# Optimization experiments

Measured on AMD Instinct MI355X. Metric: run time of the kernel, lower is better.

## Reference

```python
import jax, jax.numpy as jnp
import numpy as np

B, N, C, H = 4, 2048, 1024, 16
D = C // H  # dim_per_head = 64
NEG = -1e9  # stands in for -inf masked_fill (finite to keep grads clean)


def setup_inputs() -> dict:
    key0 = jax.random.key(0)
    ks = jax.random.split(key0, 12)
    inp = {
        "query": jax.random.normal(ks[0], (B, N, C), dtype=jnp.float32),
        "key": jax.random.normal(ks[1], (B, N, C), dtype=jnp.float32),
        "value": jax.random.normal(ks[2], (B, N, C), dtype=jnp.float32),
        "ratio": jax.random.uniform(ks[3], (B, N), dtype=jnp.float32),
        "attn_mask": jax.random.randint(ks[4], (B, N, N), 0, 2) == 1,
        # learned params (Linear layers are bias-free; weights stored as [in, out])
        "Wq": jax.random.normal(ks[5], (C, C), dtype=jnp.float32) / np.sqrt(C),
        "Wk": jax.random.normal(ks[6], (C, C), dtype=jnp.float32) / np.sqrt(C),
        "Wv": jax.random.normal(ks[7], (C, C), dtype=jnp.float32) / np.sqrt(C),
        "Wo": jax.random.normal(ks[8], (C, C), dtype=jnp.float32) / np.sqrt(C),
        "gamma": jnp.ones((C,), dtype=jnp.float32),
        "beta": jnp.zeros((C,), dtype=jnp.float32),
    }
    return inp


def reference(query, key, value, ratio, attn_mask, Wq, Wk, Wv, Wo, gamma, beta):
    residual = query
    # projections -> [B, H, N, D]
    q = (query @ Wq).reshape(B, N, H, D).transpose(0, 2, 1, 3)
    k = (key @ Wk).reshape(B, N, H, D).transpose(0, 2, 1, 3)
    v = (value @ Wv).reshape(B, N, H, D).transpose(0, 2, 1, 3)

    scale = D ** (-0.5)
    scores = jnp.einsum("bhid,bhjd->bhij", q, k) * scale  # [B,H,N1,N2]
    scores = jnp.where(attn_mask[:, None, :, :], NEG, scores)
    scores = scores * ratio[:, None, None, :]  # ratio broadcast over heads & queries
    # NON-STANDARD: softmax over dim=2 (the QUERY axis), faithful to source
    attn = jax.nn.softmax(scores, axis=2)
    # dropout omitted (eval mode)
    ctx = jnp.einsum("bhij,bhjd->bhid", attn, v)  # [B,H,N1,D]
    ctx = ctx.transpose(0, 2, 1, 3).reshape(B, N, C)
    out = ctx @ Wo
    x = residual + out
    # LayerNorm over last dim
    mu = jnp.mean(x, axis=-1, keepdims=True)
    var = jnp.var(x, axis=-1, keepdims=True)
    xn = (x - mu) * jax.lax.rsqrt(var + 1e-5)
    return xn * gamma + beta
```

## Files before the change

### kernel.cpp

```cpp
#include <hip/hip_runtime.h>
#include <hip/hip_bf16.h>
#include <stdint.h>

#define BB 4
#define NN 2048
#define CC 1024
#define HH 16
#define DD 64

typedef __attribute__((ext_vector_type(8))) short bf16x8;
typedef __attribute__((ext_vector_type(4))) float f32x4;

#define LOG2E 1.44269504088896f

__device__ __forceinline__ float exp2_hw(float x) {
  float r;
  asm("v_exp_f32 %0, %1" : "=v"(r) : "v"(x));
  return r;
}
#define EXP2(x) exp2_hw(x)

__device__ __forceinline__ unsigned short f2bf(float x) {
  uint32_t u = __float_as_uint(x);
  uint32_t r = (u + 0x7FFFu + ((u >> 16) & 1u)) >> 16;
  return (unsigned short)r;
}
__device__ __forceinline__ float bf2f(unsigned short v) {
  return __uint_as_float(((uint32_t)v) << 16);
}
__device__ __forceinline__ float load_in_f(const void* p, size_t idx, int f32in) {
  if (f32in) return ((const float*)p)[idx];
  return bf2f(((const uint16_t*)p)[idx]);
}
__device__ __forceinline__ void gload16(uint16_t* lds_base, const uint16_t* gsrc) {
  __builtin_amdgcn_global_load_lds(
      (const __attribute__((address_space(1))) uint32_t*)(const void*)gsrc,
      (__attribute__((address_space(3))) uint32_t*)(void*)lds_base,
      16, 0, 0);
}

__global__ void detect_kernel(const uint32_t* __restrict__ q,
                              const uint32_t* __restrict__ m,
                              int* __restrict__ flags) {
  if (threadIdx.x == 0 && blockIdx.x == 0) {
    int sane = 0;
    for (int i = 0; i < 128; ++i) {
      uint32_t w = q[i];
      int e0 = (int)((w >> 7) & 0xFFu);
      int e1 = (int)((w >> 23) & 0xFFu);
      sane += (e0 >= 0x70 && e0 <= 0x8F) ? 1 : 0;
      sane += (e1 >= 0x70 && e1 <= 0x8F) ? 1 : 0;
    }
    flags[0] = (sane >= 208) ? 0 : 1;
    int allsmall = 1;
    for (int i = 0; i < 16; ++i) if (m[i] > 1u) allsmall = 0;
    flags[1] = allsmall;
  }
}

__global__ void prep_kernel(const void* __restrict__ s0, const void* __restrict__ s1,
                            const void* __restrict__ s2, const void* __restrict__ ratio,
                            const void* __restrict__ mask,
                            uint16_t* __restrict__ d0, uint16_t* __restrict__ d1,
                            uint16_t* __restrict__ d2,
                            float* __restrict__ rs, float* __restrict__ ng,
                            uint32_t* __restrict__ mb, const int* __restrict__ flags) {
  const int z = blockIdx.z;
  if (z < 3) {
    const int f32in = flags[0];
    const void* src = (z == 0) ? s0 : (z == 1) ? s1 : s2;
    uint16_t* dst = (z == 0) ? d0 : (z == 1) ? d1 : d2;
    int idx = blockIdx.x * blockDim.x + threadIdx.x;
    const int total = (BB * NN * CC) >> 2;
    const int stride = gridDim.x * blockDim.x;
    if (f32in) {
      const float4* s = (const float4*)src;
      for (; idx < total; idx += stride) {
        float4 v = s[idx];
        ushort4 o;
        o.x = f2bf(v.x); o.y = f2bf(v.y); o.z = f2bf(v.z); o.w = f2bf(v.w);
        ((ushort4*)dst)[idx] = o;
      }
    } else {
      const ushort4* s = (const ushort4*)src;
      for (; idx < total; idx += stride) ((ushort4*)dst)[idx] = s[idx];
    }
  } else if (z == 3) {
    const int isint = flags[1];
    const int gw = (blockIdx.x * blockDim.x + threadIdx.x) >> 6;
    const int lane = threadIdx.x & 63;
    const int nw = (gridDim.x * blockDim.x) >> 6;
    const int totalw = (BB * NN * NN) >> 6;
    for (int w = gw; w < totalw; w += nw) {
      int e = w * 64 + lane;
      bool m;
      if (isint) m = (((const int*)mask)[e] != 0);
      else       m = (((const uint8_t*)mask)[e] != 0);
      unsigned long long bal = __ballot(m);
      if (lane == 0) ((unsigned long long*)mb)[w] = bal;
    }
  } else {
    const int f32in = flags[0];
    int idx = blockIdx.x * blockDim.x + threadIdx.x;
    if (idx < BB * NN) {
      float r = load_in_f(ratio, idx, f32in);
      rs[idx] = r * 0.125f * LOG2E;
      ng[idx] = r * (-1e9f) * LOG2E;
    }
  }
}

__global__ __launch_bounds__(256)
void transW(const void* w0, const void* w1, const void* w2, const void* w3,
            uint16_t* __restrict__ wt, const int* __restrict__ flags) {
  const int f32in = flags[0];
  const void* src = (blockIdx.z == 0) ? w0 : (blockIdx.z == 1) ? w1
                   : (blockIdx.z == 2) ? w2 : w3;
  uint16_t* dst = wt + (size_t)blockIdx.z * CC * CC;
  __shared__ float t[32][33];
  const int tx = threadIdx.x, ty = threadIdx.y;
  const int n0 = blockIdx.x * 32, k0 = blockIdx.y * 32;
#pragma unroll
  for (int r = 0; r < 4; ++r) {
    int k = k0 + ty + r * 8;
    t[ty + r * 8][tx] = load_in_f(src, (size_t)k * CC + n0 + tx, f32in);
  }
  __syncthreads();
#pragma unroll
  for (int r = 0; r < 4; ++r) {
    int n = n0 + ty + r * 8;
    dst[(size_t)n * CC + k0 + tx] = f2bf(t[tx][ty + r * 8]);
  }
}

__global__ __launch_bounds__(256, 2)
void gemmQKV(const uint16_t* __restrict__ xq, const uint16_t* __restrict__ xk,
             const uint16_t* __restrict__ xv, const uint16_t* __restrict__ Wt,
             uint16_t* __restrict__ qb, uint16_t* __restrict__ kb,
             uint16_t* __restrict__ vtb, const float* __restrict__ rowscale) {
  __shared__ uint16_t As[128 * 32];
  __shared__ uint16_t Bs[128 * 32];
  const int tid = threadIdx.x;
  const int wid = tid >> 6, lane = tid & 63;
  const int g = lane >> 4, c = lane & 15;
  const int n0g = blockIdx.y * 128;
  const int sel = n0g >> 10;
  const int n0 = n0g & 1023;
  const int m0 = blockIdx.x * 128;
  const uint16_t* A = (sel == 0) ? xq : (sel == 1) ? xk : xv;
  const uint16_t* Bt = Wt + (size_t)sel * CC * CC;
  const int wr = wid >> 1, wc = wid & 1;
  f32x4 acc[4][4] = {};
  for (int k0 = 0; k0 < 1024; k0 += 32) {
    __syncthreads();
#pragma unroll
    for (int is = 0; is < 2; ++is) {
      int sb = is * 256 + wid * 64;
      int s = sb + lane;
      int r = s >> 2, kp = s & 3;
      int kps = kp ^ ((r >> 1) & 3);
      gload16(&As[sb * 8], A + (size_t)(m0 + r) * 1024 + k0 + kps * 8);
      gload16(&Bs[sb * 8], Bt + (size_t)(n0 + r) * 1024 + k0 + kps * 8);
    }
    __syncthreads();
    bf16x8 a[4], b[4];
#pragma unroll
    for (int mi = 0; mi < 4; ++mi) {
      int row = wr * 64 + mi * 16 + c;
      a[mi] = *(const bf16x8*)&As[row * 32 + (g ^ ((row >> 1) & 3)) * 8];
    }
#pragma unroll
    for (int ni = 0; ni < 4; ++ni) {
      int row = wc * 64 + ni * 16 + c;
      b[ni] = *(const bf16x8*)&Bs[row * 32 + (g ^ ((row >> 1) & 3)) * 8];
    }
#pragma unroll
    for (int mi = 0; mi < 4; ++mi)
#pragma unroll
      for (int ni = 0; ni < 4; ++ni)
        acc[mi][ni] = __builtin_amdgcn_mfma_f32_16x16x32_bf16(a[mi], b[ni], acc[mi][ni], 0, 0, 0);
  }
  float rsv[4][4];
  if (sel == 1) {
#pragma unroll
    for (int mi = 0; mi < 4; ++mi)
#pragma unroll
      for (int r = 0; r < 4; ++r)
        rsv[mi][r] = rowscale[m0 + wr * 64 + mi * 16 + g * 4 + r];
  }
#pragma unroll
  for (int mi = 0; mi < 4; ++mi)
#pragma unroll
    for (int ni = 0; ni < 4; ++ni)
#pragma unroll
      for (int r = 0; r < 4; ++r) {
        int mrow = m0 + wr * 64 + mi * 16 + g * 4 + r;
        int ncol = n0 + wc * 64 + ni * 16 + c;
        float v = acc[mi][ni][r];
        int b_ = mrow >> 11, i = mrow & 2047, h = ncol >> 6, d = ncol & 63;
        if (sel == 0) {
          qb[((size_t)(b_ * 16 + h) * 2048 + i) * 64 + d] = f2bf(v);
        } else if (sel == 1) {
          kb[((size_t)(b_ * 16 + h) * 2048 + i) * 64 + d] = f2bf(v * rsv[mi][r]);
        } else {
          vtb[((size_t)(b_ * 16 + h) * 64 + d) * 2048 + i] = f2bf(v);
        }
      }
}

__global__ __launch_bounds__(256, 2)
void gemmO(const uint16_t* __restrict__ A, const uint16_t* __restrict__ Bt,
           float* __restrict__ out, const void* __restrict__ resid,
           const int* __restrict__ flags) {
  __shared__ uint16_t As[128 * 32];
  __shared__ uint16_t Bs[128 * 32];
  const int tid = threadIdx.x;
  const int wid = tid >> 6, lane = tid & 63;
  const int g = lane >> 4, c = lane & 15;
  const int m0 = blockIdx.x * 128, n0 = blockIdx.y * 128;
  const int wr = wid >> 1, wc = wid & 1;
  f32x4 acc[4][4] = {};
  for (int k0 = 0; k0 < 1024; k0 += 32) {
    __syncthreads();
#pragma unroll
    for (int is = 0; is < 2; ++is) {
      int sb = is * 256 + wid * 64;
      int s = sb + lane;
      int r = s >> 2, kp = s & 3;
      int kps = kp ^ ((r >> 1) & 3);
      gload16(&As[sb * 8], A + (size_t)(m0 + r) * 1024 + k0 + kps * 8);
      gload16(&Bs[sb * 8], Bt + (size_t)(n0 + r) * 1024 + k0 + kps * 8);
    }
    __syncthreads();
    bf16x8 a[4], b[4];
#pragma unroll
    for (int mi = 0; mi < 4; ++mi) {
      int row = wr * 64 + mi * 16 + c;
      a[mi] = *(const bf16x8*)&As[row * 32 + (g ^ ((row >> 1) & 3)) * 8];
    }
#pragma unroll
    for (int ni = 0; ni < 4; ++ni) {
      int row = wc * 64 + ni * 16 + c;
      b[ni] = *(const bf16x8*)&Bs[row * 32 + (g ^ ((row >> 1) & 3)) * 8];
    }
#pragma unroll
    for (int mi = 0; mi < 4; ++mi)
#pragma unroll
      for (int ni = 0; ni < 4; ++ni)
        acc[mi][ni] = __builtin_amdgcn_mfma_f32_16x16x32_bf16(a[mi], b[ni], acc[mi][ni], 0, 0, 0);
  }
  const int f32in = flags[0];
#pragma unroll
  for (int mi = 0; mi < 4; ++mi)
#pragma unroll
    for (int ni = 0; ni < 4; ++ni)
#pragma unroll
      for (int r = 0; r < 4; ++r) {
        int mrow = m0 + wr * 64 + mi * 16 + g * 4 + r;
        int ncol = n0 + wc * 64 + ni * 16 + c;
        size_t idx = (size_t)mrow * 1024 + ncol;
        out[idx] = acc[mi][ni][r] + load_in_f(resid, idx, f32in);
      }
}

__global__ __launch_bounds__(256, 2)
void attn_stats(const uint16_t* __restrict__ qb, const uint16_t* __restrict__ kb,
                uint16_t* __restrict__ vt, const uint32_t* __restrict__ mbits,
                const float* __restrict__ ngbuf) {
  __shared__ float redL[4][128];
  __shared__ float invsh[128];
  const int tid = threadIdx.x, wid = tid >> 6, lane = tid & 63;
  const int g = lane >> 4, c = lane & 15;
  const int bh = blockIdx.x, b_ = bh >> 4;
  const int j0 = blockIdx.y * 128;
  const uint16_t* Kg = kb + (size_t)bh * NN * DD + (size_t)j0 * DD;
  const uint16_t* Qg = qb + (size_t)bh * NN * DD;
  const uint32_t* Mrow = mbits + (size_t)b_ * NN * 64 + (j0 >> 5);
  bf16x8 kf[2][8];
#pragma unroll
  for (int ks = 0; ks < 2; ++ks)
#pragma unroll
    for (int nj = 0; nj < 8; ++nj)
      kf[ks][nj] = *(const bf16x8*)(Kg + (size_t)(nj * 16 + c) * 64 + ks * 32 + g * 8);
  float ng8[8], l_[8];
#pragma unroll
  for (int nj = 0; nj < 8; ++nj) {
    ng8[nj] = ngbuf[b_ * NN + j0 + nj * 16 + c];
    l_[nj] = 0.f;
  }
  bf16x8 qa[2][2], qn[2][2];
  uint4 mqa[8], mqb[8];
#pragma unroll
  for (int ks = 0; ks < 2; ++ks)
#pragma unroll
    for (int mi = 0; mi < 2; ++mi)
      qa[ks][mi] = *(const bf16x8*)(Qg + (size_t)(wid * 32 + mi * 16 + c) * 64 + ks * 32 + g * 8);
#pragma unroll
  for (int u = 0; u < 8; ++u) {
    int mi = u >> 2, r = u & 3;
    mqa[u] = *(const uint4*)(Mrow + (size_t)(wid * 32 + mi * 16 + g * 4 + r) * 64);
  }

  auto body = [&](bf16x8 (&qc)[2][2], bf16x8 (&qp)[2][2],
                  uint4 (&mc)[8], uint4 (&mn)[8], int i0) {
    f32x4 sacc[2][8] = {};
    __builtin_amdgcn_s_setprio(1);
#pragma unroll
    for (int ks = 0; ks < 2; ++ks)
#pragma unroll
      for (int mi = 0; mi < 2; ++mi)
#pragma unroll
        for (int nj = 0; nj < 8; ++nj)
          sacc[mi][nj] = __builtin_amdgcn_mfma_f32_16x16x32_bf16(qc[ks][mi], kf[ks][nj], sacc[mi][nj], 0, 0, 0);
    __builtin_amdgcn_s_setprio(0);
    int ip = (i0 + 128) & (NN - 1);
#pragma unroll
    for (int ks = 0; ks < 2; ++ks)
#pragma unroll
      for (int mi = 0; mi < 2; ++mi)
        qp[ks][mi] = *(const bf16x8*)(Qg + (size_t)(ip + wid * 32 + mi * 16 + c) * 64 + ks * 32 + g * 8);
#pragma unroll
    for (int u = 0; u < 8; ++u) {
      int mi = u >> 2, r = u & 3;
      mn[u] = *(const uint4*)(Mrow + (size_t)(ip + wid * 32 + mi * 16 + g * 4 + r) * 64);
    }
#pragma unroll
    for (int mi = 0; mi < 2; ++mi)
#pragma unroll
      for (int r = 0; r < 4; ++r) {
        const uint4 mw = mc[mi * 4 + r];
#pragma unroll
        for (int nj = 0; nj < 8; ++nj) {
          uint32_t w = (nj < 2) ? mw.x : (nj < 4) ? mw.y : (nj < 6) ? mw.z : mw.w;
          bool bit = (w >> ((nj & 1) * 16 + c)) & 1u;
          float se = bit ? ng8[nj] : sacc[mi][nj][r];
          l_[nj] += EXP2(se);
        }
      }
  };
  for (int it = 0; it < 8; ++it) {
    body(qa, qn, mqa, mqb, it * 256);
    body(qn, qa, mqb, mqa, it * 256 + 128);
  }
#pragma unroll
  for (int nj = 0; nj < 8; ++nj) {
    float l = l_[nj];
    l += __shfl_xor(l, 16);
    l += __shfl_xor(l, 32);
    if (g == 0) redL[wid][nj * 16 + c] = l;
  }
  __syncthreads();
  if (tid < 128) {
    float L = redL[0][tid] + redL[1][tid] + redL[2][tid] + redL[3][tid];
    invsh[tid] = 1.0f / L;
  }
  __syncthreads();
  {
    const int d = tid >> 2, jseg = (tid & 3) * 32;
    uint16_t* vrow = vt + (size_t)bh * DD * NN + (size_t)d * NN + j0 + jseg;
#pragma unroll
    for (int u = 0; u < 4; ++u) {
      bf16x8 v = *(const bf16x8*)(vrow + u * 8);
      bf16x8 o;
#pragma unroll
      for (int e = 0; e < 8; ++e) {
        float f = bf2f((unsigned short)v[e]) * invsh[jseg + u * 8 + e];
        o[e] = (short)f2bf(f);
      }
      *(bf16x8*)(vrow + u * 8) = o;
    }
  }
}

__global__ __launch_bounds__(256, 3)
void attn_pv(const uint16_t* __restrict__ qb, const uint16_t* __restrict__ kb,
             const uint16_t* __restrict__ vt, const uint32_t* __restrict__ mbits,
             const float* __restrict__ ngbuf, uint16_t* __restrict__ ctxr) {
  __shared__ uint16_t Ks[2][64 * 64];
  __shared__ uint16_t Vs[2][64 * 64];
  __shared__ uint16_t Ps[128 * 64];
  const int tid = threadIdx.x, wid = tid >> 6, lane = tid & 63;
  const int g = lane >> 4, c = lane & 15;
  const int bh = blockIdx.x, b_ = bh >> 4, h = bh & 15;
  const int i0 = blockIdx.y * 128;
  const uint16_t* Qg = qb + (size_t)bh * NN * DD;
  const uint16_t* Kg = kb + (size_t)bh * NN * DD;
  const uint16_t* Vg = vt + (size_t)bh * DD * NN;
  const uint32_t* Mb = mbits + (size_t)b_ * NN * 64;
  const float* ngb = ngbuf + b_ * NN;

  auto stageK = [&](int buf, int j0) {
#pragma unroll
    for (int is = 0; is < 2; ++is) {
      int sb = is * 256 + wid * 64;
      int s = sb + lane;
      int row = s >> 3, gr = s & 7;
      gload16(&Ks[buf][sb * 8], Kg + (size_t)(j0 + row) * 64 + (gr ^ (row & 7)) * 8);
    }
  };
  auto stageV = [&](int buf, int j0) {
#pragma unroll
    for (int is = 0; is < 2; ++is) {
      int sb = is * 256 + wid * 64;
      int s = sb + lane;
      int d = s >> 3, gr = s & 7;
      gload16(&Vs[buf][sb * 8], Vg + (size_t)d * NN + j0 + (gr ^ (d & 7)) * 8);
    }
  };

  bf16x8 qf[2][2];
#pragma unroll
  for (int ks = 0; ks < 2; ++ks)
#pragma unroll
    for (int mi = 0; mi < 2; ++mi)
      qf[ks][mi] = *(const bf16x8*)(Qg + (size_t)(i0 + wid * 32 + mi * 16 + c) * 64 + ks * 32 + g * 8);

  stageK(0, 0); stageV(0, 0);
  __syncthreads();

  f32x4 cacc[2][4] = {};
  for (int t = 0; t < 32; ++t) {
    const int j0 = t * 64, cb = t & 1, nb = cb ^ 1;
    if (t < 31) { stageK(nb, j0 + 64); stageV(nb, j0 + 64); }
    uint2 mw0 = *(const uint2*)(Mb + (size_t)(i0 + wid * 32 + c) * 64 + (j0 >> 5));
    uint2 mw1 = *(const uint2*)(Mb + (size_t)(i0 + wid * 32 + 16 + c) * 64 + (j0 >> 5));
    float4 ngv[4];
#pragma unroll
    for (int nj = 0; nj < 4; ++nj)
      ngv[nj] = *(const float4*)(ngb + j0 + nj * 16 + g * 4);
    f32x4 st[4][2] = {};
    __builtin_amdgcn_s_setprio(1);
#pragma unroll
    for (int ks = 0; ks < 2; ++ks) {
      bf16x8 kfr[4];
#pragma unroll
      for (int nj = 0; nj < 4; ++nj) {
        int row = nj * 16 + c;
        kfr[nj] = *(const bf16x8*)&Ks[cb][row * 64 + (((ks * 4 + g) ^ (c & 7))) * 8];
      }
#pragma unroll
      for (int nj = 0; nj < 4; ++nj)
#pragma unroll
        for (int mi = 0; mi < 2; ++mi)
          st[nj][mi] = __builtin_amdgcn_mfma_f32_16x16x32_bf16(kfr[nj], qf[ks][mi], st[nj][mi], 0, 0, 0);
    }
    __builtin_amdgcn_s_setprio(0);
    uint2 pkv[4][2];
#pragma unroll
    for (int nj = 0; nj < 4; ++nj) {
      const float4 ngq = ngv[nj];
      float nz[4] = {ngq.x, ngq.y, ngq.z, ngq.w};
#pragma unroll
      for (int mi = 0; mi < 2; ++mi) {
        const uint2 mw = mi ? mw1 : mw0;
        uint32_t w = (nj < 2) ? mw.x : mw.y;
        float p[4];
#pragma unroll
        for (int u = 0; u < 4; ++u) {
          bool bit = (w >> ((nj & 1) * 16 + g * 4 + u)) & 1u;
          float se = bit ? nz[u] : st[nj][mi][u];
          p[u] = EXP2(se);
        }
        uint32_t lo, hi;
        asm("v_cvt_pk_bf16_f32 %0, %1, %2" : "=v"(lo) : "v"(p[0]), "v"(p[1]));
        asm("v_cvt_pk_bf16_f32 %0, %1, %2" : "=v"(hi) : "v"(p[2]), "v"(p[3]));
        pkv[nj][mi] = make_uint2(lo, hi);
      }
    }
#pragma unroll
    for (int nj = 0; nj < 4; ++nj)
#pragma unroll
      for (int mi = 0; mi < 2; ++mi) {
        int iL = wid * 32 + mi * 16 + c;
        int gran = (nj * 2 + (g >> 1)) ^ (c & 7);
        *(uint2*)((char*)Ps + iL * 128 + gran * 16 + (g & 1) * 8) = pkv[nj][mi];
      }
    __syncthreads();
    __builtin_amdgcn_s_setprio(1);
#pragma unroll
    for (int ks = 0; ks < 2; ++ks) {
      bf16x8 pa[2], vb[4];
#pragma unroll
      for (int mi = 0; mi < 2; ++mi) {
        int row = wid * 32 + mi * 16 + c;
        pa[mi] = *(const bf16x8*)((const char*)Ps + row * 128 + (((ks * 4 + g) ^ (c & 7))) * 16);
      }
#pragma unroll
      for (int nd = 0; nd < 4; ++nd) {
        int row = nd * 16 + c;
        vb[nd] = *(const bf16x8*)&Vs[cb][row * 64 + (((ks * 4 + g) ^ (c & 7))) * 8];
      }
#pragma unroll
      for (int mi = 0; mi < 2; ++mi)
#pragma unroll
        for (int nd = 0; nd < 4; ++nd)
          cacc[mi][nd] = __builtin_amdgcn_mfma_f32_16x16x32_bf16(pa[mi], vb[nd], cacc[mi][nd], 0, 0, 0);
    }
    __builtin_amdgcn_s_setprio(0);
    __syncthreads();
  }
#pragma unroll
  for (int mi = 0; mi < 2; ++mi)
#pragma unroll
    for (int nd = 0; nd < 4; ++nd)
#pragma unroll
      for (int r = 0; r < 4; ++r) {
        int i = i0 + wid * 32 + mi * 16 + g * 4 + r;
        int d = nd * 16 + c;
        ctxr[((size_t)(b_ * NN + i)) * CC + h * DD + d] = f2bf(cacc[mi][nd][r]);
      }
}

__global__ __launch_bounds__(256)
void ln_kernel(const float* __restrict__ xbuf, const void* __restrict__ gamma,
               const void* __restrict__ beta, float* __restrict__ out,
               const int* __restrict__ flags) {
  const int row = blockIdx.x;
  const int tid = threadIdx.x;
  const float4 v = ((const float4*)(xbuf + (size_t)row * CC))[tid];
  float s = v.x + v.y + v.z + v.w;
  float s2 = v.x * v.x + v.y * v.y + v.z * v.z + v.w * v.w;
#pragma unroll
  for (int off = 32; off >= 1; off >>= 1) {
    s += __shfl_xor(s, off);
    s2 += __shfl_xor(s2, off);
  }
  __shared__ float red[8];
  const int wid = tid >> 6, lane = tid & 63;
  if (lane == 0) { red[wid] = s; red[4 + wid] = s2; }
  __syncthreads();
  float ts = red[0] + red[1] + red[2] + red[3];
  float ts2 = red[4] + red[5] + red[6] + red[7];
  float mu = ts * (1.f / 1024.f);
  float var = ts2 * (1.f / 1024.f) - mu * mu;
  float rs = rsqrtf(var + 1e-5f);
  const int f32in = flags[0];
  const int cbase = tid * 4;
  float4 o;
  o.x = (v.x - mu) * rs * load_in_f(gamma, cbase + 0, f32in) + load_in_f(beta, cbase + 0, f32in);
  o.y = (v.y - mu) * rs * load_in_f(gamma, cbase + 1, f32in) + load_in_f(beta, cbase + 1, f32in);
  o.z = (v.z - mu) * rs * load_in_f(gamma, cbase + 2, f32in) + load_in_f(beta, cbase + 2, f32in);
  o.w = (v.w - mu) * rs * load_in_f(gamma, cbase + 3, f32in) + load_in_f(beta, cbase + 3, f32in);
  ((float4*)(out + (size_t)row * CC))[tid] = o;
}

extern "C" void kernel_launch(void* const* d_in, const int* in_sizes, int n_in,
                              void* d_out, int out_size, void* d_ws, size_t ws_size,
                              hipStream_t stream) {
  (void)in_sizes; (void)n_in; (void)out_size; (void)ws_size;
  char* ws = (char*)d_ws;
  size_t off = 0;
  auto alloc = [&](size_t bytes) -> void* {
    void* p = ws + off;
    off += (bytes + 255) & ~(size_t)255;
    return p;
  };
  int*      flags   = (int*)alloc(256);
  float*    rsbuf   = (float*)alloc((size_t)BB * NN * 4);
  float*    ngbuf   = (float*)alloc((size_t)BB * NN * 4);
  uint32_t* mbits   = (uint32_t*)alloc((size_t)BB * NN * 64 * 4);
  uint16_t* xq      = (uint16_t*)alloc((size_t)BB * NN * CC * 2);
  uint16_t* xk      = (uint16_t*)alloc((size_t)BB * NN * CC * 2);
  uint16_t* xv      = (uint16_t*)alloc((size_t)BB * NN * CC * 2);
  uint16_t* qb      = (uint16_t*)alloc((size_t)BB * NN * CC * 2);
  uint16_t* kb      = (uint16_t*)alloc((size_t)BB * NN * CC * 2);
  uint16_t* vtb     = (uint16_t*)alloc((size_t)BB * NN * CC * 2);
  uint16_t* Wt      = (uint16_t*)alloc((size_t)4 * CC * CC * 2);
  uint16_t* ctxr    = xq;
  float*    xbuf    = (float*)xk;

  detect_kernel<<<1, 64, 0, stream>>>((const uint32_t*)d_in[0], (const uint32_t*)d_in[4], flags);
  prep_kernel<<<dim3(2048, 1, 5), 256, 0, stream>>>(d_in[0], d_in[1], d_in[2], d_in[3], d_in[4],
                                                    xq, xk, xv, rsbuf, ngbuf, mbits, flags);
  transW<<<dim3(32, 32, 4), dim3(32, 8), 0, stream>>>(d_in[5], d_in[6], d_in[7], d_in[8], Wt, flags);

  gemmQKV<<<dim3(64, 24), 256, 0, stream>>>(xq, xk, xv, Wt, qb, kb, vtb, rsbuf);

  attn_stats<<<dim3(64, 16), 256, 0, stream>>>(qb, kb, vtb, mbits, ngbuf);
  attn_pv<<<dim3(64, 16), 256, 0, stream>>>(qb, kb, vtb, mbits, ngbuf, ctxr);

  gemmO<<<dim3(64, 8), 256, 0, stream>>>(ctxr, Wt + 3 * CC * CC, xbuf, d_in[0], flags);
  ln_kernel<<<8192, 256, 0, stream>>>(xbuf, d_in[9], d_in[10], (float*)d_out, flags);
}
```

Baseline: 413.6 us.

## Load K tiles straight into registers and single-buffer V in LDS

The attention kernel stops staging K through shared memory. Each wave now loads its K fragments directly from global memory into two alternating register sets, prefetching the next tile right after the QK MFMAs. V keeps a single LDS buffer that is loaded at the start of each iteration instead of being double-buffered. A padding shared array, kept alive by a data-dependent write, holds occupancy near its previous level. The aim is to cut LDS traffic and footprint for K, at the cost of every wave re-reading K from global memory or cache and of losing the overlap of V loads with the previous tile's compute.

Measured after the change: 485.6 us. +17.4%, slower.

```diff
diff --git a/kernel.cpp b/kernel.cpp
--- a/kernel.cpp
+++ b/kernel.cpp
@@ -376,9 +376,9 @@
 void attn_pv(const uint16_t* __restrict__ qb, const uint16_t* __restrict__ kb,
              const uint16_t* __restrict__ vt, const uint32_t* __restrict__ mbits,
              const float* __restrict__ ngbuf, uint16_t* __restrict__ ctxr) {
-  __shared__ uint16_t Ks[2][64 * 64];
-  __shared__ uint16_t Vs[2][64 * 64];
+  __shared__ uint16_t Vs[64 * 64];
   __shared__ uint16_t Ps[128 * 64];
+  __shared__ uint16_t occpad[14336];
   const int tid = threadIdx.x, wid = tid >> 6, lane = tid & 63;
   const int g = lane >> 4, c = lane & 15;
   const int bh = blockIdx.x, b_ = bh >> 4, h = bh & 15;
@@ -388,24 +388,23 @@
   const uint16_t* Vg = vt + (size_t)bh * DD * NN;
   const uint32_t* Mb = mbits + (size_t)b_ * NN * 64;
   const float* ngb = ngbuf + b_ * NN;
-
-  auto stageK = [&](int buf, int j0) {
-#pragma unroll
-    for (int is = 0; is < 2; ++is) {
-      int sb = is * 256 + wid * 64;
-      int s = sb + lane;
-      int row = s >> 3, gr = s & 7;
-      gload16(&Ks[buf][sb * 8], Kg + (size_t)(j0 + row) * 64 + (gr ^ (row & 7)) * 8);
-    }
-  };
-  auto stageV = [&](int buf, int j0) {
+  if (ngb[0] > 0.5f) occpad[tid] = 1;
+
+  auto stageV = [&](int j0) {
 #pragma unroll
     for (int is = 0; is < 2; ++is) {
       int sb = is * 256 + wid * 64;
       int s = sb + lane;
       int d = s >> 3, gr = s & 7;
-      gload16(&Vs[buf][sb * 8], Vg + (size_t)d * NN + j0 + (gr ^ (d & 7)) * 8);
-    }
+      gload16(&Vs[sb * 8], Vg + (size_t)d * NN + j0 + (gr ^ (d & 7)) * 8);
+    }
+  };
+  auto loadK = [&](bf16x8 (&kf)[2][4], int j0) {
+#pragma unroll
+    for (int ks = 0; ks < 2; ++ks)
+#pragma unroll
+      for (int nj = 0; nj < 4; ++nj)
+        kf[ks][nj] = *(const bf16x8*)(Kg + (size_t)(j0 + nj * 16 + c) * 64 + ks * 32 + g * 8);
   };
 
   bf16x8 qf[2][2];
@@ -415,13 +414,13 @@
     for (int mi = 0; mi < 2; ++mi)
       qf[ks][mi] = *(const bf16x8*)(Qg + (size_t)(i0 + wid * 32 + mi * 16 + c) * 64 + ks * 32 + g * 8);
 
-  stageK(0, 0); stageV(0, 0);
-  __syncthreads();
-
+  bf16x8 kA[2][4], kB[2][4];
+  loadK(kA, 0);
   f32x4 cacc[2][4] = {};
-  for (int t = 0; t < 32; ++t) {
-    const int j0 = t * 64, cb = t & 1, nb = cb ^ 1;
-    if (t < 31) { stageK(nb, j0 + 64); stageV(nb, j0 + 64); }
+
+  auto body = [&](int t, bf16x8 (&kc)[2][4], bf16x8 (&kn)[2][4]) {
+    const int j0 = t * 64;
+    stageV(j0);
     uint2 mw0 = *(const uint2*)(Mb + (size_t)(i0 + wid * 32 + c) * 64 + (j0 >> 5));
     uint2 mw1 = *(const uint2*)(Mb + (size_t)(i0 + wid * 32 + 16 + c) * 64 + (j0 >> 5));
     float4 ngv[4];
@@ -431,20 +430,14 @@
     f32x4 st[4][2] = {};
     __builtin_amdgcn_s_setprio(1);
 #pragma unroll
-    for (int ks = 0; ks < 2; ++ks) {
-      bf16x8 kfr[4];
-#pragma unroll
-      for (int nj = 0; nj < 4; ++nj) {
-        int row = nj * 16 + c;
-        kfr[nj] = *(const bf16x8*)&Ks[cb][row * 64 + (((ks * 4 + g) ^ (c & 7))) * 8];
-      }
+    for (int ks = 0; ks < 2; ++ks)
 #pragma unroll
       for (int nj = 0; nj < 4; ++nj)
 #pragma unroll
         for (int mi = 0; mi < 2; ++mi)
-          st[nj][mi] = __builtin_amdgcn_mfma_f32_16x16x32_bf16(kfr[nj], qf[ks][mi], st[nj][mi], 0, 0, 0);
-    }
+          st[nj][mi] = __builtin_amdgcn_mfma_f32_16x16x32_bf16(kc[ks][nj], qf[ks][mi], st[nj][mi], 0, 0, 0);
     __builtin_amdgcn_s_setprio(0);
+    loadK(kn, (j0 + 64) & (NN - 1));
     uint2 pkv[4][2];
 #pragma unroll
     for (int nj = 0; nj < 4; ++nj) {
@@ -488,7 +481,7 @@
 #pragma unroll
       for (int nd = 0; nd < 4; ++nd) {
         int row = nd * 16 + c;
-        vb[nd] = *(const bf16x8*)&Vs[cb][row * 64 + (((ks * 4 + g) ^ (c & 7))) * 8];
+        vb[nd] = *(const bf16x8*)&Vs[row * 64 + (((ks * 4 + g) ^ (c & 7))) * 8];
       }
 #pragma unroll
       for (int mi = 0; mi < 2; ++mi)
@@ -498,6 +491,11 @@
     }
     __builtin_amdgcn_s_setprio(0);
     __syncthreads();
+  };
+
+  for (int tt = 0; tt < 16; ++tt) {
+    body(tt * 2, kA, kB);
+    body(tt * 2 + 1, kB, kA);
   }
 #pragma unroll
   for (int mi = 0; mi < 2; ++mi)
```
